# Optimization experiments

Measured on AMD Instinct MI355X. Metric: run time of the kernel, lower is better.

The kernel has to match this reference:

```python
import jax, jax.numpy as jnp
import numpy as np

NUM_EMBED = 8192
EMBED_DIM = 256


def setup_inputs() -> dict:
    key = jax.random.key(0)
    k1, k2 = jax.random.split(key)
    input_data = jax.random.normal(k1, (32, EMBED_DIM, 32, 32), dtype=jnp.float32)
    codebook = jax.random.normal(k2, (NUM_EMBED, EMBED_DIM), dtype=jnp.float32)
    return {"input_data": input_data, "codebook": codebook}


def reference(input_data, codebook):
    N, C, H, W = input_data.shape
    # NCHW -> NHWC -> [N*H*W, C]
    data = jnp.transpose(input_data, (0, 2, 3, 1)).reshape(-1, C)
    dist = (
        jnp.sum(data * data, axis=1, keepdims=True)          # [T, 1]
        - 2.0 * jnp.einsum("tc,kc->tk", data, codebook)      # [T, K]
        + jnp.sum(codebook * codebook, axis=1)[None, :]       # [1, K]
    )
    embed_ind = jnp.argmin(dist, axis=1)                      # [T]
    quantize = codebook[embed_ind]                            # [T, C] gather
    quantize_detach = data + jax.lax.stop_gradient(quantize - data)
    return quantize, quantize_detach, data
```

## Files before the change

kernel.cpp:

```cpp
#include <hip/hip_runtime.h>
#include <stdint.h>


#define T_TOT 32768
#define K_TOT 8192
#define CD    256
#define SPLITS 4
#define NSPLIT 2048
#define MT    64
#define NTI   32
#define BHALF 16384

typedef _Float16 h8 __attribute__((ext_vector_type(8)));
typedef _Float16 h4 __attribute__((ext_vector_type(4)));
typedef _Float16 h2 __attribute__((ext_vector_type(2)));
typedef float f4 __attribute__((ext_vector_type(4)));
typedef unsigned long long u64;
typedef unsigned int u32;

#define WS_A16   0u
#define WS_B16   16777216u
#define WS_E2    20971520u
#define WS_E2B   21004288u
#define WS_CAND  21037056u
#define WS_NEED  23265280u

__device__ __forceinline__ u64 shfl_xor_u64(u64 v, int off, int w) {
  unsigned lo = (unsigned)v, hi = (unsigned)(v >> 32);
  lo = __shfl_xor(lo, off, w);
  hi = __shfl_xor(hi, off, w);
  return ((u64)hi << 32) | lo;
}
__device__ __forceinline__ u64 umin64(u64 a, u64 b) { return a < b ? a : b; }
__device__ __forceinline__ u64 umax64(u64 a, u64 b) { return a < b ? b : a; }
__device__ __forceinline__ u32 umin32(u32 a, u32 b) { return a < b ? a : b; }
__device__ __forceinline__ u32 umax32(u32 a, u32 b) { return a < b ? b : a; }

__device__ __forceinline__ void gll16(const void* g, void* l) {
  __builtin_amdgcn_global_load_lds(
      (const __attribute__((address_space(1))) void*)g,
      (__attribute__((address_space(3))) void*)l, 16, 0, 0);
}

__device__ __forceinline__ void stage_tile(const _Float16* __restrict__ gsrc,
                                           _Float16* lbase, int w, int lane) {
  const int lrow = lane >> 5, lslot = lane & 31;
  #pragma unroll
  for (int s = 0; s < 8; ++s) {
    const int r0 = s * 8 + w * 2;
    const int r = r0 + lrow;
    const int chunk = lslot ^ (r & 7);
    gll16(gsrc + (u64)r * CD + chunk * 8, lbase + r0 * CD);
  }
}



__global__ __launch_bounds__(256) void cvt_data_kernel(
    const float* __restrict__ in, _Float16* __restrict__ A16) {
  __shared__ float Ds[32][257];
  const int tid = threadIdx.x;
  const int t0 = blockIdx.x * 32;
  const int nbase = (t0 >> 10) << 18;
  const int tin = t0 & 1023;
  #pragma unroll 8
  for (int p = 0; p < 32; ++p) {
    const int lin = p * 256 + tid;
    const int cc = lin >> 5, tt = lin & 31;
    Ds[tt][cc] = in[nbase + cc * 1024 + tin + tt];
  }
  __syncthreads();
  if (tid < 128) {
    for (int tt = 0; tt < 32; ++tt) {
      h2 hv;
      hv[0] = (_Float16)(-Ds[tt][tid * 2]);
      hv[1] = (_Float16)(-Ds[tt][tid * 2 + 1]);
      *(h2*)(A16 + (t0 + tt) * CD + tid * 2) = hv;
    }
  }
}

__global__ __launch_bounds__(256) void cvt_cb_kernel(
    const float* __restrict__ cb, _Float16* __restrict__ B16,
    float* __restrict__ e2, float* __restrict__ e2b) {
  const int tid = threadIdx.x;
  const int w = tid >> 6, lane = tid & 63;
  const int row = blockIdx.x * 4 + w;
  const float4 v = *(const float4*)(cb + row * CD + lane * 4);
  h4 hv; hv[0] = (_Float16)v.x; hv[1] = (_Float16)v.y;
  hv[2] = (_Float16)v.z; hv[3] = (_Float16)v.w;
  *(h4*)(B16 + row * CD + lane * 4) = hv;
  float s = v.x * v.x + v.y * v.y + v.z * v.z + v.w * v.w;
  #pragma unroll
  for (int off = 32; off >= 1; off >>= 1) s += __shfl_xor(s, off, 64);
  if (lane == 0) { e2[row] = s; e2b[row] = 0.5f * s + 256.0f; }
}

__global__ __launch_bounds__(256, 2) void screen_kernel(
    const _Float16* __restrict__ A, const _Float16* __restrict__ B,
    const float* __restrict__ e2b, u64* __restrict__ cand) {
  __shared__ __align__(16) _Float16 smem[2 * BHALF];

  const int tid = threadIdx.x;
  const int lane = tid & 63;
  const int w = tid >> 6;
  const int wrg = w >> 1;
  const int wcg = w & 1;
  const int q = lane >> 4;
  const int c15 = lane & 15;
  const int sx = c15 & 7;

  const int bm = blockIdx.x & 511;
  const int split = blockIdx.x >> 9;
  const int t0 = bm * MT;
  const int n0s = split * NSPLIT;

  _Float16* buf0 = smem;
  _Float16* buf1 = smem + BHALF;

  stage_tile(A + (u64)t0 * CD, buf0, w, lane);
  __syncthreads();

  h8 af[2][8];
  {
    const int m0 = wrg * 32 + c15;
    #pragma unroll
    for (int mi = 0; mi < 2; ++mi) {
      const int m = m0 + mi * 16;
      #pragma unroll
      for (int kk = 0; kk < 8; ++kk) {
        const int slot = (kk * 4 + q) ^ sx;
        af[mi][kk] = *(const h8*)(buf0 + m * CD + slot * 8);
      }
    }
  }
  stage_tile(B + (u64)n0s * CD, buf1, w, lane);

  const float* e2bs = e2b + n0s + wcg * 32 + c15;
  float ev0 = e2bs[0], ev1 = e2bs[16];

  u32 m1[8], m2[8];
  #pragma unroll
  for (int r = 0; r < 8; ++r) { m1[r] = 0xffffffffu; m2[r] = 0xffffffffu; }

  __syncthreads();

  const int nb0 = wcg * 32 + c15;
  for (int nt = 0; nt < NTI; ++nt) {
    _Float16* cur = (nt & 1) ? buf0 : buf1;
    _Float16* nxt = (nt & 1) ? buf1 : buf0;

    if (nt < NTI - 1)
      stage_tile(B + (u64)(n0s + (nt + 1) * 64) * CD, nxt, w, lane);
    const int ntn = (nt < NTI - 1) ? (nt + 1) * 64 : nt * 64;
    const float evn0 = e2bs[ntn];
    const float evn1 = e2bs[ntn + 16];

    f4 acc[2][2];
    #pragma unroll
    for (int mi = 0; mi < 2; ++mi) {
      acc[mi][0] = (f4){ev0, ev0, ev0, ev0};
      acc[mi][1] = (f4){ev1, ev1, ev1, ev1};
    }
    #pragma unroll
    for (int kk = 0; kk < 8; ++kk) {
      const int slot = (kk * 4 + q) ^ sx;
      const h8 b0 = *(const h8*)(cur + nb0 * CD + slot * 8);
      const h8 b1 = *(const h8*)(cur + (nb0 + 16) * CD + slot * 8);
      acc[0][0] = __builtin_amdgcn_mfma_f32_16x16x32_f16(af[0][kk], b0, acc[0][0], 0, 0, 0);
      acc[1][0] = __builtin_amdgcn_mfma_f32_16x16x32_f16(af[1][kk], b0, acc[1][0], 0, 0, 0);
      acc[0][1] = __builtin_amdgcn_mfma_f32_16x16x32_f16(af[0][kk], b1, acc[0][1], 0, 0, 0);
      acc[1][1] = __builtin_amdgcn_mfma_f32_16x16x32_f16(af[1][kk], b1, acc[1][1], 0, 0, 0);
    }

    #pragma unroll
    for (int mi = 0; mi < 2; ++mi)
      #pragma unroll
      for (int reg = 0; reg < 4; ++reg) {
        const int r = mi * 4 + reg;
        const u32 k0 = (__float_as_uint(acc[mi][0][reg]) & ~63u) | (u32)(nt * 2);
        const u32 k1 = (__float_as_uint(acc[mi][1][reg]) & ~63u) | (u32)(nt * 2 + 1);
        const u32 lo = umin32(k0, k1), hi = umax32(k0, k1);
        const u32 t = umax32(m1[r], lo);
        m1[r] = umin32(m1[r], lo);
        m2[r] = umin32(m2[r], umin32(hi, t));
      }
    ev0 = evn0; ev1 = evn1;
    __syncthreads();
  }

  u64 P1[8], P2[8];
  #pragma unroll
  for (int r = 0; r < 8; ++r) {
    const u32 l1 = m1[r] & 63u, l2 = m2[r] & 63u;
    const u32 col1 = (u32)(n0s + (l1 >> 1) * 64 + wcg * 32 + (l1 & 1) * 16 + c15);
    const u32 col2 = (u32)(n0s + (l2 >> 1) * 64 + wcg * 32 + (l2 & 1) * 16 + c15);
    P1[r] = ((u64)m1[r] << 32) | col1;
    P2[r] = ((u64)m2[r] << 32) | col2;
  }
  #pragma unroll
  for (int st = 1; st < 16; st <<= 1) {
    #pragma unroll
    for (int r = 0; r < 8; ++r) {
      const u64 o1 = shfl_xor_u64(P1[r], st, 16);
      const u64 o2 = shfl_xor_u64(P2[r], st, 16);
      const u64 n1 = umin64(P1[r], o1);
      const u64 hi = umax64(P1[r], o1);
      P2[r] = umin64(hi, umin64(P2[r], o2));
      P1[r] = n1;
    }
  }

  u64* mbuf = (u64*)smem;
  if (c15 == 0) {
    #pragma unroll
    for (int r = 0; r < 8; ++r) {
      const int mi = r >> 2, reg = r & 3;
      const int row = wrg * 32 + mi * 16 + q * 4 + reg;
      mbuf[(wcg * 64 + row) * 2 + 0] = P1[r];
      mbuf[(wcg * 64 + row) * 2 + 1] = P2[r];
    }
  }
  __syncthreads();
  if (tid < 64) {
    const u64 a1 = mbuf[tid * 2], a2 = mbuf[tid * 2 + 1];
    const u64 b1 = mbuf[(64 + tid) * 2], b2 = mbuf[(64 + tid) * 2 + 1];
    const u64 n1 = umin64(a1, b1);
    const u64 n2 = umin64(umax64(a1, b1), umin64(a2, b2));
    cand[(u64)(t0 + tid) * 8 + split * 2 + 0] = n1;
    cand[(u64)(t0 + tid) * 8 + split * 2 + 1] = n2;
  }
}

__global__ __launch_bounds__(256) void rescore_output_kernel(
    const float* __restrict__ in, const float* __restrict__ cb,
    const float* __restrict__ e2, const u64* __restrict__ cand,
    float* __restrict__ out) {
  __shared__ __align__(16) float Ds[32][260];
  __shared__ int idxs[32];
  const int tid = threadIdx.x;
  const int t0 = blockIdx.x * 32;
  const int nbase = (t0 >> 10) << 18;
  const int tin = t0 & 1023;
  #pragma unroll 8
  for (int p = 0; p < 32; ++p) {
    const int lin = p * 256 + tid;
    const int cc = lin >> 5, tt = lin & 31;
    Ds[tt][cc] = in[nbase + cc * 1024 + tin + tt];
  }
  __syncthreads();
  const int w = tid >> 6, lane = tid & 63;
  for (int s = 0; s < 8; ++s) {
    const int tt = w * 8 + s;
    const int t = t0 + tt;
    int colv = 0;
    if (lane < 8) colv = (int)(u32)cand[(u64)t * 8 + lane];
    const float4 x = *(const float4*)&Ds[tt][lane * 4];
    float bestd = 1e30f; int bestc = 0x7fffffff;
    #pragma unroll
    for (int j = 0; j < 8; ++j) {
      const int col = __shfl(colv, j, 64);
      const float4 e = *(const float4*)(cb + (u64)col * CD + lane * 4);
      float p4 = x.x * e.x + x.y * e.y + x.z * e.z + x.w * e.w;
      #pragma unroll
      for (int off = 32; off >= 1; off >>= 1) p4 += __shfl_xor(p4, off, 64);
      const float d = e2[col] - 2.0f * p4;
      if (d < bestd || (d == bestd && col < bestc)) { bestd = d; bestc = col; }
    }
    if (lane == 0) idxs[tt] = bestc;
  }
  __syncthreads();
  float* out1 = out;
  float* out2 = out + 8388608;
  float* out3 = out + 16777216;
  for (int tt = 0; tt < 32; ++tt) {
    const float d = Ds[tt][tid];
    const int k = idxs[tt];
    const float qv = cb[k * CD + tid];
    const float qd = d + (qv - d);
    const int o = (t0 + tt) * CD + tid;
    out1[o] = qv;
    out2[o] = qd;
    out3[o] = d;
  }
}


__global__ __launch_bounds__(256) void norms_kernel(const float* __restrict__ in,
                                                    const float* __restrict__ cb,
                                                    float* __restrict__ e2,
                                                    float* __restrict__ x2) {
  const int b = blockIdx.x;
  const int tid = threadIdx.x;
  if (b < 2048) {
    const int wave = tid >> 6, lane = tid & 63;
    const int row = b * 4 + wave;
    const float4 v = *(const float4*)(cb + row * CD + lane * 4);
    float s = v.x * v.x + v.y * v.y + v.z * v.z + v.w * v.w;
    #pragma unroll
    for (int off = 32; off >= 1; off >>= 1) s += __shfl_down(s, off, 64);
    if (lane == 0) e2[row] = s;
  } else {
    const int t = (b - 2048) * 256 + tid;
    const float* p = in + ((t >> 10) << 18) + (t & 1023);
    float s = 0.f;
    #pragma unroll 8
    for (int c = 0; c < CD; ++c) { const float v = p[c << 10]; s += v * v; }
    x2[t] = s;
  }
}

__global__ __launch_bounds__(256) void dist_argmin_kernel(
    const float* __restrict__ in, const float* __restrict__ cb,
    const float* __restrict__ e2, const float* __restrict__ x2,
    u64* __restrict__ packed) {
  __shared__ __align__(16) float As_[32][128];
  __shared__ __align__(16) float Bs_[32][128];
  const int tid = threadIdx.x;
  const int tx = tid & 15, ty = tid >> 4;
  const int tb = blockIdx.x & 255;
  const int ks = blockIdx.x >> 8;
  const int t0 = tb * 128;
  const int nbase = (t0 >> 10) << 18;
  const int tin = t0 & 1023;
  float xi[8];
  #pragma unroll
  for (int i = 0; i < 8; ++i)
    xi[i] = x2[t0 + ty * 4 + (i & 3) + ((i >> 2) << 6)];
  u64 best[8];
  #pragma unroll
  for (int i = 0; i < 8; ++i) best[i] = ~0ull;
  for (int kt = 0; kt < 32; ++kt) {
    const int k0 = ks * 4096 + kt * 128;
    float acc[8][8];
    #pragma unroll
    for (int i = 0; i < 8; ++i)
      #pragma unroll
      for (int j = 0; j < 8; ++j) acc[i][j] = 0.f;
    float ej[8];
    #pragma unroll
    for (int j = 0; j < 8; ++j)
      ej[j] = e2[k0 + tx * 4 + (j & 3) + ((j >> 2) << 6)];
    for (int ch = 0; ch < 8; ++ch) {
      const int c0 = ch * 32;
      #pragma unroll
      for (int p = 0; p < 4; ++p) {
        const int l = p * 1024 + tid * 4;
        const int cc = l >> 7, tt = l & 127;
        *(float4*)&As_[cc][tt] =
            *(const float4*)(in + nbase + (c0 + cc) * 1024 + tin + tt);
      }
      #pragma unroll
      for (int p = 0; p < 4; ++p) {
        const int ix = p * 256 + tid;
        const int kk = ix >> 3, cs = (ix & 7) * 4;
        const float4 v = *(const float4*)(cb + (k0 + kk) * CD + c0 + cs);
        Bs_[cs + 0][kk] = v.x; Bs_[cs + 1][kk] = v.y;
        Bs_[cs + 2][kk] = v.z; Bs_[cs + 3][kk] = v.w;
      }
      __syncthreads();
      #pragma unroll
      for (int cc = 0; cc < 32; ++cc) {
        const float4 a0 = *(const float4*)&As_[cc][ty * 4];
        const float4 a1 = *(const float4*)&As_[cc][64 + ty * 4];
        const float4 b0 = *(const float4*)&Bs_[cc][tx * 4];
        const float4 b1 = *(const float4*)&Bs_[cc][64 + tx * 4];
        const float a[8]  = {a0.x, a0.y, a0.z, a0.w, a1.x, a1.y, a1.z, a1.w};
        const float bb[8] = {b0.x, b0.y, b0.z, b0.w, b1.x, b1.y, b1.z, b1.w};
        #pragma unroll
        for (int i = 0; i < 8; ++i)
          #pragma unroll
          for (int j = 0; j < 8; ++j)
            acc[i][j] += a[i] * bb[j];
      }
      __syncthreads();
    }
    #pragma unroll
    for (int i = 0; i < 8; ++i) {
      u64 m = best[i];
      #pragma unroll
      for (int j = 0; j < 8; ++j) {
        const float dist = (xi[i] - 2.0f * acc[i][j]) + ej[j];
        const int kidx = k0 + tx * 4 + (j & 3) + ((j >> 2) << 6);
        const u64 pk = ((u64)__float_as_uint(dist) << 32) | (unsigned)kidx;
        m = pk < m ? pk : m;
      }
      best[i] = m;
    }
  }
  #pragma unroll
  for (int i = 0; i < 8; ++i) {
    u64 m = best[i];
    #pragma unroll
    for (int off = 8; off >= 1; off >>= 1) {
      const u64 o = shfl_xor_u64(m, off, 16);
      m = o < m ? o : m;
    }
    if (tx == 0)
      atomicMin(&packed[t0 + ty * 4 + (i & 3) + ((i >> 2) << 6)], m);
  }
}

__global__ __launch_bounds__(256) void output_kernel(
    const float* __restrict__ in, const float* __restrict__ cb,
    const u64* __restrict__ packed, float* __restrict__ out) {
  __shared__ float Ds[32][257];
  __shared__ int idxs[32];
  const int tid = threadIdx.x;
  const int t0 = blockIdx.x * 32;
  const int nbase = (t0 >> 10) << 18;
  const int tin = t0 & 1023;
  if (tid < 32) idxs[tid] = (int)(packed[t0 + tid] & 0xffffffffull);
  #pragma unroll 8
  for (int p = 0; p < 32; ++p) {
    const int lin = p * 256 + tid;
    const int cc = lin >> 5, tt = lin & 31;
    Ds[tt][cc] = in[nbase + cc * 1024 + tin + tt];
  }
  __syncthreads();
  float* out1 = out;
  float* out2 = out + 8388608;
  float* out3 = out + 16777216;
  for (int tt = 0; tt < 32; ++tt) {
    const float d = Ds[tt][tid];
    const int k = idxs[tt];
    const float q = cb[k * CD + tid];
    const float qd = d + (q - d);
    const int o = (t0 + tt) * CD + tid;
    out1[o] = q;
    out2[o] = qd;
    out3[o] = d;
  }
}

extern "C" void kernel_launch(void* const* d_in, const int* in_sizes, int n_in,
                              void* d_out, int out_size, void* d_ws, size_t ws_size,
                              hipStream_t stream) {
  const float* in = (const float*)d_in[0];
  const float* cb = (const float*)d_in[1];
  float* out = (float*)d_out;

  if (ws_size >= WS_NEED) {
    _Float16* A16 = (_Float16*)((char*)d_ws + WS_A16);
    _Float16* B16 = (_Float16*)((char*)d_ws + WS_B16);
    float* e2  = (float*)((char*)d_ws + WS_E2);
    float* e2b = (float*)((char*)d_ws + WS_E2B);
    u64* cand  = (u64*)((char*)d_ws + WS_CAND);

    cvt_data_kernel<<<T_TOT / 32, 256, 0, stream>>>(in, A16);
    cvt_cb_kernel<<<K_TOT / 4, 256, 0, stream>>>(cb, B16, e2, e2b);
    screen_kernel<<<(T_TOT / MT) * SPLITS, 256, 0, stream>>>(A16, B16, e2b, cand);
    rescore_output_kernel<<<T_TOT / 32, 256, 0, stream>>>(in, cb, e2, cand, out);
  } else {
    u64* packed = (u64*)d_ws;
    float* e2 = (float*)((char*)d_ws + 262144);
    float* x2 = (float*)((char*)d_ws + 294912);
    hipMemsetAsync(packed, 0xFF, T_TOT * sizeof(u64), stream);
    norms_kernel<<<2176, 256, 0, stream>>>(in, cb, e2, x2);
    dist_argmin_kernel<<<512, 256, 0, stream>>>(in, cb, e2, x2, packed);
    output_kernel<<<T_TOT / 32, 256, 0, stream>>>(in, cb, packed, out);
  }
}
```

Baseline: 336.5 us.

## Pre-tile fp16 operands into MFMA-fragment layout and write transposed data once

The conversion kernels now write A and B in a per-64-row tile layout that matches the MFMA fragment order. Each tile can then be staged with contiguous global-to-LDS loads, without the XOR swizzle. The screen kernel changes its wave layout so that each wave holds all 64 token rows and one 16-column slice. This needs a single B fragment load per k-step and one candidate key per tile, but doubles the A-fragment and top-2 register state. The transposed fp32 data output is now written by the conversion kernel and read back contiguously by the rescore kernel, which no longer re-transposes the NCHW input; the input load in the conversion kernel is also vectorised.

Result: slower. 361.8 us (+7.5%).

```diff
diff --git a/kernel.cpp b/kernel.cpp
--- a/kernel.cpp
+++ b/kernel.cpp
@@ -9,17 +9,16 @@
 #define NSPLIT 2048
 #define MT    64
 #define NTI   32
-#define BHALF 16384
+#define TILEH 16384
 
 typedef _Float16 h8 __attribute__((ext_vector_type(8)));
 typedef _Float16 h4 __attribute__((ext_vector_type(4)));
-typedef _Float16 h2 __attribute__((ext_vector_type(2)));
 typedef float f4 __attribute__((ext_vector_type(4)));
 typedef unsigned long long u64;
 typedef unsigned int u32;
 
-#define WS_A16   0u
-#define WS_B16   16777216u
+#define WS_AFT   0u
+#define WS_BFT   16777216u
 #define WS_E2    20971520u
 #define WS_E2B   21004288u
 #define WS_CAND  21037056u
@@ -42,166 +41,175 @@
       (__attribute__((address_space(3))) void*)l, 16, 0, 0);
 }
 
-__device__ __forceinline__ void stage_tile(const _Float16* __restrict__ gsrc,
-                                           _Float16* lbase, int w, int lane) {
-  const int lrow = lane >> 5, lslot = lane & 31;
-  #pragma unroll
-  for (int s = 0; s < 8; ++s) {
-    const int r0 = s * 8 + w * 2;
-    const int r = r0 + lrow;
-    const int chunk = lslot ^ (r & 7);
-    gll16(gsrc + (u64)r * CD + chunk * 8, lbase + r0 * CD);
-  }
-}
-
 
 
 __global__ __launch_bounds__(256) void cvt_data_kernel(
-    const float* __restrict__ in, _Float16* __restrict__ A16) {
+    const float* __restrict__ in, _Float16* __restrict__ Aft,
+    float* __restrict__ out3) {
   __shared__ float Ds[32][257];
   const int tid = threadIdx.x;
   const int t0 = blockIdx.x * 32;
   const int nbase = (t0 >> 10) << 18;
   const int tin = t0 & 1023;
+
+  #pragma unroll
+  for (int p = 0; p < 8; ++p) {
+    const int item = p * 256 + tid;
+    const int cc = item >> 3, t4 = (item & 7) * 4;
+    const float4 v = *(const float4*)(in + nbase + cc * 1024 + tin + t4);
+    Ds[t4 + 0][cc] = v.x; Ds[t4 + 1][cc] = v.y;
+    Ds[t4 + 2][cc] = v.z; Ds[t4 + 3][cc] = v.w;
+  }
+  __syncthreads();
+
   #pragma unroll 8
-  for (int p = 0; p < 32; ++p) {
-    const int lin = p * 256 + tid;
-    const int cc = lin >> 5, tt = lin & 31;
-    Ds[tt][cc] = in[nbase + cc * 1024 + tin + tt];
-  }
-  __syncthreads();
-  if (tid < 128) {
-    for (int tt = 0; tt < 32; ++tt) {
-      h2 hv;
-      hv[0] = (_Float16)(-Ds[tt][tid * 2]);
-      hv[1] = (_Float16)(-Ds[tt][tid * 2 + 1]);
-      *(h2*)(A16 + (t0 + tt) * CD + tid * 2) = hv;
-    }
+  for (int tt = 0; tt < 32; ++tt)
+    out3[(u64)(t0 + tt) * CD + tid] = Ds[tt][tid];
+
+  const u64 tbase = (u64)(t0 >> 6) * TILEH + (u64)(t0 & 63) * 8;
+  #pragma unroll
+  for (int p = 0; p < 4; ++p) {
+    const int item = p * 256 + tid;
+    const int s = item >> 5, tt = item & 31;
+    h8 hv;
+    #pragma unroll
+    for (int j = 0; j < 8; ++j) hv[j] = (_Float16)(-Ds[tt][s * 8 + j]);
+    *(h8*)(Aft + tbase + s * 512 + tt * 8) = hv;
   }
 }
 
 __global__ __launch_bounds__(256) void cvt_cb_kernel(
-    const float* __restrict__ cb, _Float16* __restrict__ B16,
+    const float* __restrict__ cb, _Float16* __restrict__ Bft,
     float* __restrict__ e2, float* __restrict__ e2b) {
   const int tid = threadIdx.x;
   const int w = tid >> 6, lane = tid & 63;
-  const int row = blockIdx.x * 4 + w;
-  const float4 v = *(const float4*)(cb + row * CD + lane * 4);
-  h4 hv; hv[0] = (_Float16)v.x; hv[1] = (_Float16)v.y;
-  hv[2] = (_Float16)v.z; hv[3] = (_Float16)v.w;
-  *(h4*)(B16 + row * CD + lane * 4) = hv;
-  float s = v.x * v.x + v.y * v.y + v.z * v.z + v.w * v.w;
-  #pragma unroll
-  for (int off = 32; off >= 1; off >>= 1) s += __shfl_xor(s, off, 64);
-  if (lane == 0) { e2[row] = s; e2b[row] = 0.5f * s + 256.0f; }
+  const int tile = blockIdx.x;
+  const int c0 = tile * 64;
+  const int s = lane >> 1, off4 = (lane & 1) * 4;
+  #pragma unroll 4
+  for (int i = 0; i < 16; ++i) {
+    const int r = i * 4 + w;
+    const float4 v = *(const float4*)(cb + (u64)(c0 + r) * CD + lane * 4);
+    h4 hv; hv[0] = (_Float16)v.x; hv[1] = (_Float16)v.y;
+    hv[2] = (_Float16)v.z; hv[3] = (_Float16)v.w;
+    *(h4*)(Bft + (u64)tile * TILEH + s * 512 + r * 8 + off4) = hv;
+    float sum = v.x * v.x + v.y * v.y + v.z * v.z + v.w * v.w;
+    #pragma unroll
+    for (int o = 32; o >= 1; o >>= 1) sum += __shfl_xor(sum, o, 64);
+    if (lane == 0) { e2[c0 + r] = sum; e2b[c0 + r] = 0.5f * sum + 256.0f; }
+  }
 }
 
 __global__ __launch_bounds__(256, 2) void screen_kernel(
-    const _Float16* __restrict__ A, const _Float16* __restrict__ B,
+    const _Float16* __restrict__ Aft, const _Float16* __restrict__ Bft,
     const float* __restrict__ e2b, u64* __restrict__ cand) {
-  __shared__ __align__(16) _Float16 smem[2 * BHALF];
+  __shared__ __align__(16) _Float16 smem[2 * TILEH];
 
   const int tid = threadIdx.x;
   const int lane = tid & 63;
   const int w = tid >> 6;
-  const int wrg = w >> 1;
-  const int wcg = w & 1;
   const int q = lane >> 4;
   const int c15 = lane & 15;
-  const int sx = c15 & 7;
 
   const int bm = blockIdx.x & 511;
   const int split = blockIdx.x >> 9;
   const int t0 = bm * MT;
   const int n0s = split * NSPLIT;
+  const int btile0 = split * NTI;
 
   _Float16* buf0 = smem;
-  _Float16* buf1 = smem + BHALF;
-
-  stage_tile(A + (u64)t0 * CD, buf0, w, lane);
-  __syncthreads();
-
-  h8 af[2][8];
+  _Float16* buf1 = smem + TILEH;
+
   {
-    const int m0 = wrg * 32 + c15;
-    #pragma unroll
-    for (int mi = 0; mi < 2; ++mi) {
-      const int m = m0 + mi * 16;
-      #pragma unroll
-      for (int kk = 0; kk < 8; ++kk) {
-        const int slot = (kk * 4 + q) ^ sx;
-        af[mi][kk] = *(const h8*)(buf0 + m * CD + slot * 8);
-      }
-    }
-  }
-  stage_tile(B + (u64)n0s * CD, buf1, w, lane);
-
-  const float* e2bs = e2b + n0s + wcg * 32 + c15;
-  float ev0 = e2bs[0], ev1 = e2bs[16];
-
-  u32 m1[8], m2[8];
-  #pragma unroll
-  for (int r = 0; r < 8; ++r) { m1[r] = 0xffffffffu; m2[r] = 0xffffffffu; }
-
-  __syncthreads();
-
-  const int nb0 = wcg * 32 + c15;
+    const _Float16* Atile = Aft + (u64)bm * TILEH;
+    #pragma unroll
+    for (int ii = 0; ii < 8; ++ii) {
+      const int i = w * 8 + ii;
+      gll16(Atile + i * 512 + lane * 8, buf0 + i * 512);
+    }
+  }
+  __syncthreads();
+
+  h8 af[4][8];
+  #pragma unroll
+  for (int mi = 0; mi < 4; ++mi) {
+    const int m = mi * 16 + c15;
+    #pragma unroll
+    for (int kk = 0; kk < 8; ++kk)
+      af[mi][kk] = *(const h8*)(buf0 + (kk * 4 + q) * 512 + m * 8);
+  }
+
+  {
+    const _Float16* Btile = Bft + (u64)btile0 * TILEH;
+    #pragma unroll
+    for (int ii = 0; ii < 8; ++ii) {
+      const int i = w * 8 + ii;
+      gll16(Btile + i * 512 + lane * 8, buf1 + i * 512);
+    }
+  }
+
+  const float* e2bs = e2b + n0s + w * 16 + c15;
+  float ev = e2bs[0];
+
+  u32 m1[16], m2[16];
+  #pragma unroll
+  for (int r = 0; r < 16; ++r) { m1[r] = 0xffffffffu; m2[r] = 0xffffffffu; }
+
+  __syncthreads();
+
+  const int nb8 = (w * 16 + c15) * 8;
   for (int nt = 0; nt < NTI; ++nt) {
     _Float16* cur = (nt & 1) ? buf0 : buf1;
     _Float16* nxt = (nt & 1) ? buf1 : buf0;
 
-    if (nt < NTI - 1)
-      stage_tile(B + (u64)(n0s + (nt + 1) * 64) * CD, nxt, w, lane);
-    const int ntn = (nt < NTI - 1) ? (nt + 1) * 64 : nt * 64;
-    const float evn0 = e2bs[ntn];
-    const float evn1 = e2bs[ntn + 16];
-
-    f4 acc[2][2];
-    #pragma unroll
-    for (int mi = 0; mi < 2; ++mi) {
-      acc[mi][0] = (f4){ev0, ev0, ev0, ev0};
-      acc[mi][1] = (f4){ev1, ev1, ev1, ev1};
-    }
+    if (nt < NTI - 1) {
+      const _Float16* Btile = Bft + (u64)(btile0 + nt + 1) * TILEH;
+      #pragma unroll
+      for (int ii = 0; ii < 8; ++ii) {
+        const int i = w * 8 + ii;
+        gll16(Btile + i * 512 + lane * 8, nxt + i * 512);
+      }
+    }
+    const float evn = e2bs[(nt < NTI - 1 ? nt + 1 : nt) * 64];
+
+    f4 acc[4];
+    #pragma unroll
+    for (int mi = 0; mi < 4; ++mi) acc[mi] = (f4){ev, ev, ev, ev};
+
     #pragma unroll
     for (int kk = 0; kk < 8; ++kk) {
-      const int slot = (kk * 4 + q) ^ sx;
-      const h8 b0 = *(const h8*)(cur + nb0 * CD + slot * 8);
-      const h8 b1 = *(const h8*)(cur + (nb0 + 16) * CD + slot * 8);
-      acc[0][0] = __builtin_amdgcn_mfma_f32_16x16x32_f16(af[0][kk], b0, acc[0][0], 0, 0, 0);
-      acc[1][0] = __builtin_amdgcn_mfma_f32_16x16x32_f16(af[1][kk], b0, acc[1][0], 0, 0, 0);
-      acc[0][1] = __builtin_amdgcn_mfma_f32_16x16x32_f16(af[0][kk], b1, acc[0][1], 0, 0, 0);
-      acc[1][1] = __builtin_amdgcn_mfma_f32_16x16x32_f16(af[1][kk], b1, acc[1][1], 0, 0, 0);
-    }
-
-    #pragma unroll
-    for (int mi = 0; mi < 2; ++mi)
+      const h8 bf = *(const h8*)(cur + (kk * 4 + q) * 512 + nb8);
+      acc[0] = __builtin_amdgcn_mfma_f32_16x16x32_f16(af[0][kk], bf, acc[0], 0, 0, 0);
+      acc[1] = __builtin_amdgcn_mfma_f32_16x16x32_f16(af[1][kk], bf, acc[1], 0, 0, 0);
+      acc[2] = __builtin_amdgcn_mfma_f32_16x16x32_f16(af[2][kk], bf, acc[2], 0, 0, 0);
+      acc[3] = __builtin_amdgcn_mfma_f32_16x16x32_f16(af[3][kk], bf, acc[3], 0, 0, 0);
+    }
+
+    #pragma unroll
+    for (int mi = 0; mi < 4; ++mi)
       #pragma unroll
       for (int reg = 0; reg < 4; ++reg) {
         const int r = mi * 4 + reg;
-        const u32 k0 = (__float_as_uint(acc[mi][0][reg]) & ~63u) | (u32)(nt * 2);
-        const u32 k1 = (__float_as_uint(acc[mi][1][reg]) & ~63u) | (u32)(nt * 2 + 1);
-        const u32 lo = umin32(k0, k1), hi = umax32(k0, k1);
-        const u32 t = umax32(m1[r], lo);
-        m1[r] = umin32(m1[r], lo);
-        m2[r] = umin32(m2[r], umin32(hi, t));
-      }
-    ev0 = evn0; ev1 = evn1;
+        const u32 key = (__float_as_uint(acc[mi][reg]) & ~63u) | (u32)nt;
+        const u32 t = umax32(m1[r], key);
+        m1[r] = umin32(m1[r], key);
+        m2[r] = umin32(m2[r], t);
+      }
+    ev = evn;
     __syncthreads();
   }
 
-  u64 P1[8], P2[8];
-  #pragma unroll
-  for (int r = 0; r < 8; ++r) {
-    const u32 l1 = m1[r] & 63u, l2 = m2[r] & 63u;
-    const u32 col1 = (u32)(n0s + (l1 >> 1) * 64 + wcg * 32 + (l1 & 1) * 16 + c15);
-    const u32 col2 = (u32)(n0s + (l2 >> 1) * 64 + wcg * 32 + (l2 & 1) * 16 + c15);
-    P1[r] = ((u64)m1[r] << 32) | col1;
-    P2[r] = ((u64)m2[r] << 32) | col2;
+  const u32 cbase = (u32)(n0s + w * 16 + c15);
+  u64 P1[16], P2[16];
+  #pragma unroll
+  for (int r = 0; r < 16; ++r) {
+    P1[r] = ((u64)m1[r] << 32) | (cbase + ((m1[r] & 63u) << 6));
+    P2[r] = ((u64)m2[r] << 32) | (cbase + ((m2[r] & 63u) << 6));
   }
   #pragma unroll
   for (int st = 1; st < 16; st <<= 1) {
     #pragma unroll
-    for (int r = 0; r < 8; ++r) {
+    for (int r = 0; r < 16; ++r) {
       const u64 o1 = shfl_xor_u64(P1[r], st, 16);
       const u64 o2 = shfl_xor_u64(P2[r], st, 16);
       const u64 n1 = umin64(P1[r], o1);
@@ -214,39 +222,42 @@
   u64* mbuf = (u64*)smem;
   if (c15 == 0) {
     #pragma unroll
-    for (int r = 0; r < 8; ++r) {
-      const int mi = r >> 2, reg = r & 3;
-      const int row = wrg * 32 + mi * 16 + q * 4 + reg;
-      mbuf[(wcg * 64 + row) * 2 + 0] = P1[r];
-      mbuf[(wcg * 64 + row) * 2 + 1] = P2[r];
+    for (int r = 0; r < 16; ++r) {
+      const int token = (r >> 2) * 16 + q * 4 + (r & 3);
+      mbuf[(w * 64 + token) * 2 + 0] = P1[r];
+      mbuf[(w * 64 + token) * 2 + 1] = P2[r];
     }
   }
   __syncthreads();
   if (tid < 64) {
-    const u64 a1 = mbuf[tid * 2], a2 = mbuf[tid * 2 + 1];
-    const u64 b1 = mbuf[(64 + tid) * 2], b2 = mbuf[(64 + tid) * 2 + 1];
-    const u64 n1 = umin64(a1, b1);
-    const u64 n2 = umin64(umax64(a1, b1), umin64(a2, b2));
-    cand[(u64)(t0 + tid) * 8 + split * 2 + 0] = n1;
-    cand[(u64)(t0 + tid) * 8 + split * 2 + 1] = n2;
+    u64 a1 = mbuf[tid * 2], a2 = mbuf[tid * 2 + 1];
+    #pragma unroll
+    for (int ww = 1; ww < 4; ++ww) {
+      const u64 b1 = mbuf[(ww * 64 + tid) * 2];
+      const u64 b2 = mbuf[(ww * 64 + tid) * 2 + 1];
+      const u64 n1 = umin64(a1, b1);
+      a2 = umin64(umax64(a1, b1), umin64(a2, b2));
+      a1 = n1;
+    }
+    cand[(u64)(t0 + tid) * 8 + split * 2 + 0] = a1;
+    cand[(u64)(t0 + tid) * 8 + split * 2 + 1] = a2;
   }
 }
 
 __global__ __launch_bounds__(256) void rescore_output_kernel(
-    const float* __restrict__ in, const float* __restrict__ cb,
+    const float* __restrict__ out3, const float* __restrict__ cb,
     const float* __restrict__ e2, const u64* __restrict__ cand,
     float* __restrict__ out) {
   __shared__ __align__(16) float Ds[32][260];
   __shared__ int idxs[32];
   const int tid = threadIdx.x;
   const int t0 = blockIdx.x * 32;
-  const int nbase = (t0 >> 10) << 18;
-  const int tin = t0 & 1023;
-  #pragma unroll 8
-  for (int p = 0; p < 32; ++p) {
-    const int lin = p * 256 + tid;
-    const int cc = lin >> 5, tt = lin & 31;
-    Ds[tt][cc] = in[nbase + cc * 1024 + tin + tt];
+  #pragma unroll
+  for (int p = 0; p < 8; ++p) {
+    const int item = p * 256 + tid;
+    const int tt = item >> 6, c4 = (item & 63) * 4;
+    const float4 v = *(const float4*)(out3 + (u64)(t0 + tt) * CD + c4);
+    *(float4*)&Ds[tt][c4] = v;
   }
   __syncthreads();
   const int w = tid >> 6, lane = tid & 63;
@@ -272,16 +283,14 @@
   __syncthreads();
   float* out1 = out;
   float* out2 = out + 8388608;
-  float* out3 = out + 16777216;
   for (int tt = 0; tt < 32; ++tt) {
     const float d = Ds[tt][tid];
     const int k = idxs[tt];
-    const float qv = cb[k * CD + tid];
+    const float qv = cb[(u64)k * CD + tid];
     const float qd = d + (qv - d);
     const int o = (t0 + tt) * CD + tid;
     out1[o] = qv;
     out2[o] = qd;
-    out3[o] = d;
   }
 }
 
@@ -441,16 +450,17 @@
   float* out = (float*)d_out;
 
   if (ws_size >= WS_NEED) {
-    _Float16* A16 = (_Float16*)((char*)d_ws + WS_A16);
-    _Float16* B16 = (_Float16*)((char*)d_ws + WS_B16);
+    _Float16* Aft = (_Float16*)((char*)d_ws + WS_AFT);
+    _Float16* Bft = (_Float16*)((char*)d_ws + WS_BFT);
     float* e2  = (float*)((char*)d_ws + WS_E2);
     float* e2b = (float*)((char*)d_ws + WS_E2B);
     u64* cand  = (u64*)((char*)d_ws + WS_CAND);
-
-    cvt_data_kernel<<<T_TOT / 32, 256, 0, stream>>>(in, A16);
-    cvt_cb_kernel<<<K_TOT / 4, 256, 0, stream>>>(cb, B16, e2, e2b);
-    screen_kernel<<<(T_TOT / MT) * SPLITS, 256, 0, stream>>>(A16, B16, e2b, cand);
-    rescore_output_kernel<<<T_TOT / 32, 256, 0, stream>>>(in, cb, e2, cand, out);
+    float* out3 = out + 16777216;
+
+    cvt_data_kernel<<<T_TOT / 32, 256, 0, stream>>>(in, Aft, out3);
+    cvt_cb_kernel<<<K_TOT / 64, 256, 0, stream>>>(cb, Bft, e2, e2b);
+    screen_kernel<<<(T_TOT / MT) * SPLITS, 256, 0, stream>>>(Aft, Bft, e2b, cand);
+    rescore_output_kernel<<<T_TOT / 32, 256, 0, stream>>>(out3, cb, e2, cand, out);
   } else {
     u64* packed = (u64*)d_ws;
     float* e2 = (float*)((char*)d_ws + 262144);
```
